# Performance work log

Hardware: AMD Instinct MI355X
Metric: run time of the kernel (lower is better)

Reference implementation:

```python
import jax, jax.numpy as jnp
import numpy as np


def _dsepconv(inp, vert, horiz, offx, offy, mask):
    # inp: [B,C,H,W]; vert/horiz: [B,F,H,W]; offx/offy/mask: [B,F*F,H,W]
    B, C, H, W = inp.shape
    F = vert.shape[1]
    FF = F * F
    dt = inp.dtype
    k = jnp.arange(FF)
    ki = (k // F).astype(dt)   # vertical tap index i
    kj = (k % F).astype(dt)    # horizontal tap index j
    half = jnp.asarray((F - 1) / 2.0, dt)
    ys = jnp.arange(H, dtype=dt)
    xs = jnp.arange(W, dtype=dt)
    # per-pixel deformable sample positions, [B,FF,H,W]
    py = offy + ys[None, None, :, None] + (ki - half)[None, :, None, None]
    px = offx + xs[None, None, None, :] + (kj - half)[None, :, None, None]
    py = jnp.clip(py, 0.0, H - 1)
    px = jnp.clip(px, 0.0, W - 1)
    y0f = jnp.floor(py)
    x0f = jnp.floor(px)
    wy = py - y0f   # bilinear fractional weights
    wx = px - x0f
    y0 = y0f.astype(jnp.int32)
    x0 = x0f.astype(jnp.int32)
    y1 = jnp.minimum(y0 + 1, H - 1)
    x1 = jnp.minimum(x0 + 1, W - 1)

    inp_flat = inp.reshape(B, C, H * W)

    def gather(yi, xi):
        # flat spatial gather per batch element -> [B,C,FF,H,W]
        idx = (yi * W + xi).reshape(B, FF * H * W)
        g = jax.vmap(lambda im, ix: im[:, ix])(inp_flat, idx)
        return g.reshape(B, C, FF, H, W)

    g00 = gather(y0, x0)
    g01 = gather(y0, x1)
    g10 = gather(y1, x0)
    g11 = gather(y1, x1)
    wy_ = wy[:, None]  # [B,1,FF,H,W]
    wx_ = wx[:, None]
    samp = (g00 * (1 - wy_) * (1 - wx_)
            + g01 * (1 - wy_) * wx_
            + g10 * wy_ * (1 - wx_)
            + g11 * wy_ * wx_)  # [B,C,FF,H,W]
    # separable mask-weighted tap weights: vert[i]*horiz[j]*mask[k]
    wtap = vert[:, k // F] * horiz[:, k % F] * mask  # [B,FF,H,W]
    return jnp.einsum('bkhw,bckhw->bchw', wtap, samp)


def setup_inputs() -> dict:
    key = jax.random.key(0)
    ks = jax.random.split(key, 6)
    B, C, H, W, F = 4, 3, 384, 384, 5
    return {
        'tensorInput': jax.random.normal(ks[0], (B, C, H, W), jnp.float32),
        'tensorVertical': jax.random.uniform(ks[1], (B, F, H, W), jnp.float32),
        'tensorHorizontal': jax.random.uniform(ks[2], (B, F, H, W), jnp.float32),
        'tensorOffsetX': jax.random.normal(ks[3], (B, F * F, H, W), jnp.float32),
        'tensorOffsetY': jax.random.normal(ks[4], (B, F * F, H, W), jnp.float32),
        'tensorMask': jax.random.uniform(ks[5], (B, F * F, H, W), jnp.float32),
    }


def reference(tensorInput, tensorVertical, tensorHorizontal, tensorOffsetX, tensorOffsetY, tensorMask):
    return _dsepconv(tensorInput, tensorVertical, tensorHorizontal,
                     tensorOffsetX, tensorOffsetY, tensorMask)
```

## Files before the change

### kernel.cpp

```cpp
#include <hip/hip_runtime.h>
#include <hip/hip_fp16.h>

#define BB 4
#define CC 3
#define HH 384
#define WW 384
#define FF 5
#define KK 25
#define HW (HH*WW)

#define TX 64
#define TY 8
#define MX 10
#define MY 9
#define RH 28
#define RWC 86
#define C2S 178
#define C2N (RH*RWC)
#define LDSW (RH*C2S)

typedef float fx2 __attribute__((ext_vector_type(2)));

__device__ __forceinline__ fx2 nt_load2(const float* p) {
    return __builtin_nontemporal_load((const fx2*)p);
}
__device__ __forceinline__ unsigned h2bits(__half2 h) {
    return *(const unsigned int*)&h;
}

__global__ __launch_bounds__(256) void pack_kernel(
    const float* __restrict__ inp, uint4* __restrict__ qtab)
{
    int t = blockIdx.x * blockDim.x + threadIdx.x;
    if (t >= BB * HW) return;
    int b   = t / HW;
    int rem = t - b * HW;
    int y   = rem / WW;
    int x   = rem - y * WW;
    int x1  = min(x + 1, WW - 1);
    int yn  = min(y + 1, HH - 1);
    const float* c0p = inp + (size_t)b * CC * HW;
    const float* c1p = c0p + HW;
    int o00 = y * WW + x,  o01 = y * WW + x1;
    int o10 = yn * WW + x, o11 = yn * WW + x1;
    qtab[t] = make_uint4(
        h2bits(__floats2half2_rn(c0p[o00], c1p[o00])),
        h2bits(__floats2half2_rn(c0p[o01], c1p[o01])),
        h2bits(__floats2half2_rn(c0p[o10], c1p[o10])),
        h2bits(__floats2half2_rn(c0p[o11], c1p[o11])));
}

__global__ __launch_bounds__(256) void dsepconv_kernel(
    const uint4* __restrict__ qtab,
    const float* __restrict__ inp,
    const float* __restrict__ vert,
    const float* __restrict__ horiz,
    const float* __restrict__ offx,
    const float* __restrict__ offy,
    const float* __restrict__ mask,
    float* __restrict__ out)
{
    __shared__ unsigned int ldsw[LDSW];

    int tx = threadIdx.x & 31;
    int ty = threadIdx.x >> 5;
    int X  = blockIdx.x * TX;
    int Y  = blockIdx.y * TY;
    int xb = X + tx * 2;
    int y  = Y + ty;
    int b  = blockIdx.z;
    int ylo = Y - MY, xlo = X - MX;
    int planeoff = y * WW + xb;

    const float* c2p = inp + ((size_t)b * CC + 2) * HW;

    for (int p = threadIdx.x; p < C2N; p += 256) {
        int r = p / RWC;
        int c = p - r * RWC;
        int gy  = min(max(ylo + r, 0), HH - 1);
        int gy1 = min(gy + 1, HH - 1);
        int gx  = min(max(xlo + c, 0), WW - 1);
        int gx1 = min(gx + 1, WW - 1);
        float v00 = c2p[gy * WW + gx],  v01 = c2p[gy * WW + gx1];
        float v10 = c2p[gy1 * WW + gx], v11 = c2p[gy1 * WW + gx1];
        int o = r * C2S + c * 2;
        ldsw[o]     = h2bits(__floats2half2_rn(v00, v01));
        ldsw[o + 1] = h2bits(__floats2half2_rn(v10, v11));
    }
    __syncthreads();

    fx2 v2[FF], h2[FF];
#pragma unroll
    for (int f = 0; f < FF; ++f) {
        v2[f] = nt_load2(vert  + (b * FF + f) * HW + planeoff);
        h2[f] = nt_load2(horiz + (b * FF + f) * HW + planeoff);
    }

    const uint4* qt = qtab + (size_t)b * HW;

    float acc[2][3] = {{0.f,0.f,0.f},{0.f,0.f,0.f}};
    const float fy = (float)y;

    for (int ki = 0; ki < FF; ++ki) {
        float dy = fy + (float)(ki - 2);
        const float* ox_p = offx + (size_t)(b * KK + ki * FF) * HW + planeoff;
        const float* oy_p = offy + (size_t)(b * KK + ki * FF) * HW + planeoff;
        const float* m_p  = mask + (size_t)(b * KK + ki * FF) * HW + planeoff;
#pragma unroll
        for (int kj = 0; kj < FF; ++kj) {
            fx2 ox2 = nt_load2(ox_p + kj * HW);
            fx2 oy2 = nt_load2(oy_p + kj * HW);
            fx2 m2  = nt_load2(m_p  + kj * HW);
#pragma unroll
            for (int p = 0; p < 2; ++p) {
                float wt = v2[ki][p] * h2[kj][p] * m2[p];
                float py = oy2[p] + dy;
                float px = ox2[p] + (float)(xb + p + kj - 2);
                py = fminf(fmaxf(py, 0.f), (float)(HH - 1));
                px = fminf(fmaxf(px, 0.f), (float)(WW - 1));
                float y0f = floorf(py);
                float x0f = floorf(px);
                float wy = py - y0f;
                float wx = px - x0f;
                int y0 = (int)y0f;
                int x0 = (int)x0f;

                uint4 g = qt[y0 * WW + x0];
                float2 f00 = __half22float2(*(const __half2*)&g.x);
                float2 f01 = __half22float2(*(const __half2*)&g.y);
                float2 f10 = __half22float2(*(const __half2*)&g.z);
                float2 f11 = __half22float2(*(const __half2*)&g.w);

                int y0r = y0 - ylo;
                int x0r = x0 - xlo;
                bool ok = ((unsigned)y0r <= (unsigned)(RH - 1)) &
                          ((unsigned)x0r <= (unsigned)(RWC - 1));
                int yc = min(max(y0r, 0), RH - 1);
                int xc = min(max(x0r, 0), RWC - 1);
                const unsigned int* sp = &ldsw[yc * C2S + xc * 2];
                unsigned s0 = sp[0], s1 = sp[1];
                float2 c2a = __half22float2(*(const __half2*)&s0);
                float2 c2b = __half22float2(*(const __half2*)&s1);
                float s00c2 = c2a.x, s01c2 = c2a.y;
                float s10c2 = c2b.x, s11c2 = c2b.y;

                if (__builtin_expect(!__all((int)ok), 0)) {
                    if (!ok) {
                        int x1  = min(x0 + 1, WW - 1);
                        int y1g = min(y0 + 1, HH - 1);
                        s00c2 = c2p[y0 * WW + x0];
                        s01c2 = c2p[y0 * WW + x1];
                        s10c2 = c2p[y1g * WW + x0];
                        s11c2 = c2p[y1g * WW + x1];
                    }
                }

                float w00 = (1.f - wy) * (1.f - wx);
                float w01 = (1.f - wy) * wx;
                float w10 = wy * (1.f - wx);
                float w11 = wy * wx;

                acc[p][0] += wt * (f00.x*w00 + f01.x*w01 + f10.x*w10 + f11.x*w11);
                acc[p][1] += wt * (f00.y*w00 + f01.y*w01 + f10.y*w10 + f11.y*w11);
                acc[p][2] += wt * (s00c2*w00 + s01c2*w01 + s10c2*w10 + s11c2*w11);
            }
        }
    }

#pragma unroll
    for (int c = 0; c < CC; ++c) {
        fx2 o; o.x = acc[0][c]; o.y = acc[1][c];
        *(fx2*)(out + ((size_t)b * CC + c) * HW + planeoff) = o;
    }
}

extern "C" void kernel_launch(void* const* d_in, const int* in_sizes, int n_in,
                              void* d_out, int out_size, void* d_ws, size_t ws_size,
                              hipStream_t stream) {
    const float* inp   = (const float*)d_in[0];
    const float* vert  = (const float*)d_in[1];
    const float* horiz = (const float*)d_in[2];
    const float* offx  = (const float*)d_in[3];
    const float* offy  = (const float*)d_in[4];
    const float* mask  = (const float*)d_in[5];
    float* out = (float*)d_out;
    uint4* qtab = (uint4*)d_ws;

    {
        pack_kernel<<<(BB * HW + 255) / 256, 256, 0, stream>>>(inp, qtab);
    }
    {
        dim3 grid(WW / TX, HH / TY, BB);
        dsepconv_kernel<<<grid, 256, 0, stream>>>(
            qtab, inp, vert, horiz, offx, offy, mask, out);
    }
}
```

Measured before the change: 239.7 us.

## Pack all three channels into a 32-byte global table, drop LDS staging

Channel 2's bilinear corners move into the packed global table, so each entry is 32 bytes (16-byte channels 0/1 quad plus an 8-byte channel-2 pair) instead of 16 bytes. The dsepconv kernel drops its shared-memory tile of channel 2, the __syncthreads, and the out-of-tile fallback path, so every tap is served by one 32-byte gather. This removes LDS fill cost and divergent fallback loads, but doubles the workspace table and the gather footprint per tap, which relies on cache hits.

```diff
diff --git a/kernel.cpp b/kernel.cpp
--- a/kernel.cpp
+++ b/kernel.cpp
@@ -11,13 +11,6 @@
 
 #define TX 64
 #define TY 8
-#define MX 10
-#define MY 9
-#define RH 28
-#define RWC 86
-#define C2S 178
-#define C2N (RH*RWC)
-#define LDSW (RH*C2S)
 
 typedef float fx2 __attribute__((ext_vector_type(2)));
 
@@ -29,7 +22,7 @@
 }
 
 __global__ __launch_bounds__(256) void pack_kernel(
-    const float* __restrict__ inp, uint4* __restrict__ qtab)
+    const float* __restrict__ inp, uint2* __restrict__ qtab)
 {
     int t = blockIdx.x * blockDim.x + threadIdx.x;
     if (t >= BB * HW) return;
@@ -41,18 +34,23 @@
     int yn  = min(y + 1, HH - 1);
     const float* c0p = inp + (size_t)b * CC * HW;
     const float* c1p = c0p + HW;
+    const float* c2p = c1p + HW;
     int o00 = y * WW + x,  o01 = y * WW + x1;
     int o10 = yn * WW + x, o11 = yn * WW + x1;
-    qtab[t] = make_uint4(
-        h2bits(__floats2half2_rn(c0p[o00], c1p[o00])),
-        h2bits(__floats2half2_rn(c0p[o01], c1p[o01])),
-        h2bits(__floats2half2_rn(c0p[o10], c1p[o10])),
-        h2bits(__floats2half2_rn(c0p[o11], c1p[o11])));
+    unsigned d0 = h2bits(__floats2half2_rn(c0p[o00], c1p[o00]));
+    unsigned d1 = h2bits(__floats2half2_rn(c0p[o01], c1p[o01]));
+    unsigned d2 = h2bits(__floats2half2_rn(c0p[o10], c1p[o10]));
+    unsigned d3 = h2bits(__floats2half2_rn(c0p[o11], c1p[o11]));
+    unsigned d4 = h2bits(__floats2half2_rn(c2p[o00], c2p[o01]));
+    unsigned d5 = h2bits(__floats2half2_rn(c2p[o10], c2p[o11]));
+    uint2* e = qtab + ((size_t)t << 2);
+    e[0] = make_uint2(d0, d1);
+    e[1] = make_uint2(d2, d3);
+    e[2] = make_uint2(d4, d5);
 }
 
 __global__ __launch_bounds__(256) void dsepconv_kernel(
-    const uint4* __restrict__ qtab,
-    const float* __restrict__ inp,
+    const uint2* __restrict__ qtab,
     const float* __restrict__ vert,
     const float* __restrict__ horiz,
     const float* __restrict__ offx,
@@ -60,34 +58,12 @@
     const float* __restrict__ mask,
     float* __restrict__ out)
 {
-    __shared__ unsigned int ldsw[LDSW];
-
     int tx = threadIdx.x & 31;
     int ty = threadIdx.x >> 5;
-    int X  = blockIdx.x * TX;
-    int Y  = blockIdx.y * TY;
-    int xb = X + tx * 2;
-    int y  = Y + ty;
+    int xb = blockIdx.x * TX + tx * 2;
+    int y  = blockIdx.y * TY + ty;
     int b  = blockIdx.z;
-    int ylo = Y - MY, xlo = X - MX;
     int planeoff = y * WW + xb;
-
-    const float* c2p = inp + ((size_t)b * CC + 2) * HW;
-
-    for (int p = threadIdx.x; p < C2N; p += 256) {
-        int r = p / RWC;
-        int c = p - r * RWC;
-        int gy  = min(max(ylo + r, 0), HH - 1);
-        int gy1 = min(gy + 1, HH - 1);
-        int gx  = min(max(xlo + c, 0), WW - 1);
-        int gx1 = min(gx + 1, WW - 1);
-        float v00 = c2p[gy * WW + gx],  v01 = c2p[gy * WW + gx1];
-        float v10 = c2p[gy1 * WW + gx], v11 = c2p[gy1 * WW + gx1];
-        int o = r * C2S + c * 2;
-        ldsw[o]     = h2bits(__floats2half2_rn(v00, v01));
-        ldsw[o + 1] = h2bits(__floats2half2_rn(v10, v11));
-    }
-    __syncthreads();
 
     fx2 v2[FF], h2[FF];
 #pragma unroll
@@ -96,7 +72,7 @@
         h2[f] = nt_load2(horiz + (b * FF + f) * HW + planeoff);
     }
 
-    const uint4* qt = qtab + (size_t)b * HW;
+    const uint2* qt = qtab + ((size_t)b * HW << 2);
 
     float acc[2][3] = {{0.f,0.f,0.f},{0.f,0.f,0.f}};
     const float fy = (float)y;
@@ -125,35 +101,16 @@
                 int y0 = (int)y0f;
                 int x0 = (int)x0f;
 
-                uint4 g = qt[y0 * WW + x0];
+                const uint2* ep = qt + ((size_t)(y0 * WW + x0) << 2);
+                uint4 g  = *(const uint4*)ep;
+                uint2 g2 = ep[2];
+
                 float2 f00 = __half22float2(*(const __half2*)&g.x);
                 float2 f01 = __half22float2(*(const __half2*)&g.y);
                 float2 f10 = __half22float2(*(const __half2*)&g.z);
                 float2 f11 = __half22float2(*(const __half2*)&g.w);
-
-                int y0r = y0 - ylo;
-                int x0r = x0 - xlo;
-                bool ok = ((unsigned)y0r <= (unsigned)(RH - 1)) &
-                          ((unsigned)x0r <= (unsigned)(RWC - 1));
-                int yc = min(max(y0r, 0), RH - 1);
-                int xc = min(max(x0r, 0), RWC - 1);
-                const unsigned int* sp = &ldsw[yc * C2S + xc * 2];
-                unsigned s0 = sp[0], s1 = sp[1];
-                float2 c2a = __half22float2(*(const __half2*)&s0);
-                float2 c2b = __half22float2(*(const __half2*)&s1);
-                float s00c2 = c2a.x, s01c2 = c2a.y;
-                float s10c2 = c2b.x, s11c2 = c2b.y;
-
-                if (__builtin_expect(!__all((int)ok), 0)) {
-                    if (!ok) {
-                        int x1  = min(x0 + 1, WW - 1);
-                        int y1g = min(y0 + 1, HH - 1);
-                        s00c2 = c2p[y0 * WW + x0];
-                        s01c2 = c2p[y0 * WW + x1];
-                        s10c2 = c2p[y1g * WW + x0];
-                        s11c2 = c2p[y1g * WW + x1];
-                    }
-                }
+                float2 c2a = __half22float2(*(const __half2*)&g2.x);
+                float2 c2b = __half22float2(*(const __half2*)&g2.y);
 
                 float w00 = (1.f - wy) * (1.f - wx);
                 float w01 = (1.f - wy) * wx;
@@ -162,7 +119,7 @@
 
                 acc[p][0] += wt * (f00.x*w00 + f01.x*w01 + f10.x*w10 + f11.x*w11);
                 acc[p][1] += wt * (f00.y*w00 + f01.y*w01 + f10.y*w10 + f11.y*w11);
-                acc[p][2] += wt * (s00c2*w00 + s01c2*w01 + s10c2*w10 + s11c2*w11);
+                acc[p][2] += wt * (c2a.x*w00 + c2a.y*w01 + c2b.x*w10 + c2b.y*w11);
             }
         }
     }
@@ -184,7 +141,7 @@
     const float* offy  = (const float*)d_in[4];
     const float* mask  = (const float*)d_in[5];
     float* out = (float*)d_out;
-    uint4* qtab = (uint4*)d_ws;
+    uint2* qtab = (uint2*)d_ws;
 
     {
         pack_kernel<<<(BB * HW + 255) / 256, 256, 0, stream>>>(inp, qtab);
@@ -192,6 +149,6 @@
     {
         dim3 grid(WW / TX, HH / TY, BB);
         dsepconv_kernel<<<grid, 256, 0, stream>>>(
-            qtab, inp, vert, horiz, offx, offy, mask, out);
+            qtab, vert, horiz, offx, offy, mask, out);
     }
 }
```

Measured after the change: 244.0 us. About the same (+1.8%).
